# Performance work log

Measured on AMD Instinct MI355X. Metric: run time of the kernel, lower is better.

The kernel has to match this reference:

```python
import jax, jax.numpy as jnp
import numpy as np

B, D_IN, D_H, D_OUT, E = 8192, 512, 2048, 512, 8


def setup_inputs() -> dict:
    key = jax.random.key(0)
    k = jax.random.split(key, 6)
    return {
        "x": jax.random.normal(k[0], (B, D_IN), dtype=jnp.float32),
        "groups": jax.random.randint(k[1], (B, 1), 0, E, dtype=jnp.int64),
        "W1": jax.random.normal(k[2], (E, D_IN, D_H), dtype=jnp.float32) * (1.0 / np.sqrt(D_IN)),
        "b1": jnp.zeros((E, D_H), dtype=jnp.float32),
        "W2": jax.random.normal(k[3], (E, D_H, D_OUT), dtype=jnp.float32) * (1.0 / np.sqrt(D_H)),
        "b2": jnp.zeros((E, D_OUT), dtype=jnp.float32),
    }


def reference(x, groups, W1, b1, W2, b2):
    # SubnetGate: hard one-hot routing on group column 0, then weighted
    # combine (gate value is exactly 1.0 for the selected expert).
    n_expert = W1.shape[0]
    gate = jax.nn.one_hot(groups[:, 0], n_expert, dtype=x.dtype)  # [B, E]
    out = jnp.zeros((x.shape[0], W2.shape[-1]), dtype=x.dtype)
    # Loop over the small fixed expert set (structurally distinct subnets);
    # mask-combine reproduces dispatch -> subnet -> scatter/combine exactly.
    for e in range(n_expert):
        h = jax.nn.relu(x @ W1[e] + b1[e])        # [B, D_H]
        y = h @ W2[e] + b2[e]                      # [B, D_OUT]
        out = out + gate[:, e:e + 1] * y
    return out
```

## Files before the change

kernel.cpp:

```cpp
#include <hip/hip_runtime.h>
#include <hip/hip_bf16.h>

typedef unsigned short u16;
typedef __bf16 bf16x8 __attribute__((ext_vector_type(8)));
typedef float floatx4 __attribute__((ext_vector_type(4)));
typedef unsigned short ushort8 __attribute__((ext_vector_type(8)));

#define GLOBAL_AS(p) ((const __attribute__((address_space(1))) void*)(p))
#define LDS_AS(p) ((__attribute__((address_space(3))) void*)(p))

constexpr int NB = 8192;
constexpr int DIN = 512;
constexpr int DH = 2048;
constexpr int DOUT = 512;
constexpr int NEXP = 8;
constexpr int ROWCAP = NB + NEXP * 128;
constexpr int RCAPRD = NB + NEXP * 256;
constexpr int TILE = 8192;

__device__ __forceinline__ u16 f2bf(float f) {
    unsigned u = __builtin_bit_cast(unsigned, f);
    unsigned r = u + 0x7FFFu + ((u >> 16) & 1u);
    return (u16)(r >> 16);
}

__device__ __forceinline__ int slot_off(int row, int kl) {
    return row * 64 + ((((kl >> 3) ^ (row & 7)) << 3) | (kl & 7));
}

__global__ __launch_bounds__(1024) void route_kernel(
        const int* __restrict__ groups, int* __restrict__ cnt,
        int* __restrict__ offs, int* __restrict__ perm, int* __restrict__ rpos) {
    __shared__ int wc[NEXP * 16];
    __shared__ int lcur[NEXP * 16];
    int t = threadIdx.x;
    int w = t >> 6;
    if (t < NEXP * 16) wc[t] = 0;
    __syncthreads();
    for (int i = t; i < NB; i += 1024) atomicAdd(&wc[groups[i] * 16 + w], 1);
    __syncthreads();
    if (t == 0) {
        int run = 0;
        for (int e = 0; e < NEXP; ++e) {
            offs[e] = run;
            int s = run;
            for (int j = 0; j < 16; ++j) { lcur[e * 16 + j] = s; s += wc[e * 16 + j]; }
            cnt[e] = s - run;
            run += (((s - run) + 127) >> 7) << 7;
        }
    }
    __syncthreads();
    for (int i = t; i < NB; i += 1024) {
        int e = groups[i];
        int pos = atomicAdd(&lcur[e * 16 + w], 1);
        perm[pos] = i;
        rpos[i] = pos;
    }
}

__global__ __launch_bounds__(256) void prep_kernel(
        const float* __restrict__ x, const float* __restrict__ W1,
        const float* __restrict__ W2, const int* __restrict__ rpos,
        u16* __restrict__ xsT, u16* __restrict__ w1tT, u16* __restrict__ w2tT) {
    int bx = blockIdx.x;
    int t = threadIdx.x;
    if (bx < 4096) {
        __shared__ float tile[64][65];
        bool isW1 = bx < 2048;
        int b = isW1 ? bx : bx - 2048;
        int e = b >> 8;
        int q = b & 255;
        int C = isW1 ? DH : DOUT;
        int NTP = C >> 7;
        int KTP = isW1 ? (DIN >> 6) : (DH >> 6);
        int rt = isW1 ? (q >> 5) : (q >> 3);
        int ct = isW1 ? (q & 31) : (q & 7);
        const float* s = (isW1 ? W1 : W2) + (size_t)e * (isW1 ? DIN * DH : DH * DOUT);
        u16* d = isW1 ? w1tT : w2tT;
        int r0 = rt * 64, c0 = ct * 64;
        for (int i = 0; i < 4; ++i) {
            int r = (t >> 4) + i * 16;
            int c = (t & 15) * 4;
            const float4 v = *(const float4*)&s[(size_t)(r0 + r) * C + c0 + c];
            tile[r][c] = v.x; tile[r][c + 1] = v.y; tile[r][c + 2] = v.z; tile[r][c + 3] = v.w;
        }
        __syncthreads();
        for (int i = 0; i < 2; ++i) {
            int c = (t >> 3) + i * 32;
            int r = (t & 7) * 8;
            int n = c0 + c, k = r0 + r;
            ushort8 o;
#pragma unroll
            for (int j = 0; j < 8; ++j) o[j] = f2bf(tile[r + j][c]);
            size_t off = ((size_t)(e * NTP + (n >> 7)) * KTP + (k >> 6)) * TILE
                         + slot_off(n & 127, k & 63);
            *(ushort8*)&d[off] = o;
        }
    } else {
        int r = t >> 6, lane = t & 63;
        int i = (bx - 4096) * 4 + r;
        int pos = rpos[i];
        int k = lane * 8;
        const float4 a = *(const float4*)&x[(size_t)i * DIN + k];
        const float4 b = *(const float4*)&x[(size_t)i * DIN + k + 4];
        ushort8 o;
        o[0] = f2bf(a.x); o[1] = f2bf(a.y); o[2] = f2bf(a.z); o[3] = f2bf(a.w);
        o[4] = f2bf(b.x); o[5] = f2bf(b.y); o[6] = f2bf(b.z); o[7] = f2bf(b.w);
        int lp = pos & 127;
        size_t off = (size_t)(pos >> 7) * 8 * TILE + (size_t)(k >> 6) * TILE
                     + slot_off(lp, k & 63);
        *(ushort8*)&xsT[off] = o;
    }
}


#define LDF(base, row, c0) \
    (*(const bf16x8*)&(base)[(row) * 64 + ((((c0) ^ ((row) & 7))) << 3)])

__device__ __forceinline__ void stage3(const u16* a0, const u16* a1, const u16* b,
                                       u16* buf, int soff, int doff) {
    __builtin_amdgcn_global_load_lds(GLOBAL_AS(a0 + soff), LDS_AS(buf + doff), 16, 0, 0);
    __builtin_amdgcn_global_load_lds(GLOBAL_AS(a0 + 4096 + soff), LDS_AS(buf + 4096 + doff), 16, 0, 0);
    __builtin_amdgcn_global_load_lds(GLOBAL_AS(a1 + soff), LDS_AS(buf + TILE + doff), 16, 0, 0);
    __builtin_amdgcn_global_load_lds(GLOBAL_AS(a1 + 4096 + soff), LDS_AS(buf + TILE + 4096 + doff), 16, 0, 0);
    __builtin_amdgcn_global_load_lds(GLOBAL_AS(b + soff), LDS_AS(buf + 2 * TILE + doff), 16, 0, 0);
    __builtin_amdgcn_global_load_lds(GLOBAL_AS(b + 4096 + soff), LDS_AS(buf + 2 * TILE + 4096 + doff), 16, 0, 0);
}

__device__ __forceinline__ void compute_step(const u16* At, const u16* Bt,
                                             int arow, int brow,
                                             floatx4 (&acc)[4][4], int q, int li) {
#pragma unroll
    for (int s = 0; s < 2; ++s) {
        int c0 = s * 4 + q;
        bf16x8 bfr[4];
#pragma unroll
        for (int fn = 0; fn < 4; ++fn) bfr[fn] = LDF(Bt, brow + fn * 16 + li, c0);
#pragma unroll
        for (int fm = 0; fm < 4; ++fm) {
            bf16x8 af = LDF(At, arow + fm * 16 + li, c0);
#pragma unroll
            for (int fn = 0; fn < 4; ++fn)
                acc[fm][fn] = __builtin_amdgcn_mfma_f32_16x16x32_bf16(
                    af, bfr[fn], acc[fm][fn], 0, 0, 0);
        }
    }
}

template <int KT>
__device__ __forceinline__ void gemm_core3(const u16* a0, const u16* a1, const u16* b0,
                                           u16* sm, floatx4 (&acc)[4][4],
                                           int aslot, int arow, int brow,
                                           int q, int li, int soff, int doff) {
    stage3(a0, a1, b0, sm, soff, doff);
    stage3(a0 + TILE, a1 + TILE, b0 + TILE, sm + 3 * TILE, soff, doff);
    int cur = 0;
#pragma unroll 1
    for (int kt = 0; kt < KT; ++kt) {
        if (kt + 2 < KT) {
            int nb = cur + 2; if (nb >= 3) nb -= 3;
            stage3(a0 + (size_t)(kt + 2) * TILE, a1 + (size_t)(kt + 2) * TILE,
                   b0 + (size_t)(kt + 2) * TILE, sm + (size_t)nb * 3 * TILE, soff, doff);
            asm volatile("s_waitcnt vmcnt(12)" ::: "memory");
        } else if (kt + 1 < KT) {
            asm volatile("s_waitcnt vmcnt(6)" ::: "memory");
        } else {
            asm volatile("s_waitcnt vmcnt(0)" ::: "memory");
        }
        __builtin_amdgcn_s_barrier();
        __builtin_amdgcn_sched_barrier(0);
        const u16* At = sm + (size_t)(cur * 3 + aslot) * TILE;
        const u16* Bt = sm + (size_t)(cur * 3 + 2) * TILE;
        compute_step(At, Bt, arow, brow, acc, q, li);
        __builtin_amdgcn_s_barrier();
        cur = (cur == 2) ? 0 : cur + 1;
    }
}

__global__ __launch_bounds__(512) __attribute__((amdgpu_waves_per_eu(2)))
void gemm_a(const u16* __restrict__ At, const u16* __restrict__ Bt,
            const float* __restrict__ bias, u16* __restrict__ hsT,
            const int* __restrict__ cnt, const int* __restrict__ offs) {
    __shared__ u16 sm[3 * 3 * TILE];
    int bx = blockIdx.x;
    int e = bx & 7;
    int r = bx >> 3;
    int nt = r & 15;
    int mt0 = r >> 4;
    int count = cnt[e];
    int base128 = offs[e] >> 7;
    int tid = threadIdx.x;
    int w = tid >> 6, l = tid & 63, q = l >> 4, li = l & 15;
    int wm = w >> 1, wn = w & 1;
    int aslot = wm >> 1, arow = (wm & 1) * 64, brow = wn * 64;
    int soff = tid * 8, doff = w * 512;
#pragma unroll 1
    for (int mt = mt0; mt * 256 < count; mt += 5) {
        const u16* a0 = At + (size_t)((base128 + mt * 2 + 0) * 8) * TILE;
        const u16* a1 = At + (size_t)((base128 + mt * 2 + 1) * 8) * TILE;
        const u16* b0 = Bt + (size_t)((e * 16 + nt) * 8) * TILE;
        floatx4 acc[4][4];
#pragma unroll
        for (int a = 0; a < 4; ++a)
#pragma unroll
            for (int b = 0; b < 4; ++b) acc[a][b] = (floatx4)0.0f;

        gemm_core3<8>(a0, a1, b0, sm, acc, aslot, arow, brow, q, li, soff, doff);

        float bv[4];
#pragma unroll
        for (int fn = 0; fn < 4; ++fn)
            bv[fn] = bias[(size_t)e * DH + nt * 128 + wn * 64 + fn * 16 + li];
        u16* img = sm + (size_t)w * 4096;
#pragma unroll
        for (int fm = 0; fm < 4; ++fm)
#pragma unroll
            for (int fn = 0; fn < 4; ++fn)
#pragma unroll
                for (int rr = 0; rr < 4; ++rr) {
                    float v = acc[fm][fn][rr] + bv[fn];
                    v = v > 0.0f ? v : 0.0f;
                    int row = fm * 16 + q * 4 + rr;
                    int col = fn * 16 + li;
                    img[row * 64 + ((((col >> 3) ^ (row & 7)) << 3) | (col & 7))] = f2bf(v);
                }
        if ((mt * 2 + aslot) * 128 < count) {
            u16* dst = hsT + ((size_t)(base128 + mt * 2 + aslot) * 32 + nt * 2 + wn) * TILE
                       + (wm & 1) * 4096;
#pragma unroll
            for (int j = 0; j < 8; ++j)
                *(ushort8*)&dst[j * 512 + l * 8] = *(const ushort8*)&img[j * 512 + l * 8];
        }
        __syncthreads();
    }
}

__global__ __launch_bounds__(512) __attribute__((amdgpu_waves_per_eu(2)))
void gemm_b(const u16* __restrict__ At, const u16* __restrict__ Bt,
            float* __restrict__ ps, const int* __restrict__ cnt,
            const int* __restrict__ offs) {
    __shared__ u16 sm[3 * 3 * TILE];
    int bx = blockIdx.x;
    int e = bx & 7;
    int r = bx >> 3;
    int nt = r & 3;
    int ks = (r >> 2) & 1;
    int mt0 = r >> 3;
    int count = cnt[e];
    int seg = offs[e];
    int base128 = seg >> 7;
    int tid = threadIdx.x;
    int w = tid >> 6, l = tid & 63, q = l >> 4, li = l & 15;
    int wm = w >> 1, wn = w & 1;
    int aslot = wm >> 1, arow = (wm & 1) * 64, brow = wn * 64;
    int soff = tid * 8, doff = w * 512;
#pragma unroll 1
    for (int mt = mt0; mt * 256 < count; mt += 5) {
        const u16* a0 = At + (size_t)((base128 + mt * 2 + 0) * 32 + ks * 16) * TILE;
        const u16* a1 = At + (size_t)((base128 + mt * 2 + 1) * 32 + ks * 16) * TILE;
        const u16* b0 = Bt + (size_t)((e * 4 + nt) * 32 + ks * 16) * TILE;
        floatx4 acc[4][4];
#pragma unroll
        for (int a = 0; a < 4; ++a)
#pragma unroll
            for (int b = 0; b < 4; ++b) acc[a][b] = (floatx4)0.0f;

        gemm_core3<16>(a0, a1, b0, sm, acc, aslot, arow, brow, q, li, soff, doff);

        if ((mt * 2 + aslot) * 128 < count) {
            float* pbase = ps + ((size_t)ks * ROWCAP + seg + (size_t)mt * 256) * DOUT;
#pragma unroll
            for (int fn = 0; fn < 4; ++fn) {
                int col = nt * 128 + wn * 64 + fn * 16 + li;
#pragma unroll
                for (int fm = 0; fm < 4; ++fm) {
                    int row0 = wm * 64 + fm * 16 + q * 4;
#pragma unroll
                    for (int rr = 0; rr < 4; ++rr)
                        pbase[(size_t)(row0 + rr) * DOUT + col] = acc[fm][fn][rr];
                }
            }
        }
        __syncthreads();
    }
}

__global__ __launch_bounds__(256) void reduce_b(
        const float* __restrict__ ps, const int* __restrict__ rpos,
        const int* __restrict__ groups, const float* __restrict__ b2,
        float* __restrict__ out) {
    int idx = blockIdx.x * 256 + threadIdx.x;
    int i = idx >> 7;
    int c = (idx & 127) * 4;
    int pos = rpos[i];
    int g = groups[i];
    const float4 v0 = *(const float4*)&ps[(size_t)pos * DOUT + c];
    const float4 v1 = *(const float4*)&ps[((size_t)ROWCAP + pos) * DOUT + c];
    const float4 bb = *(const float4*)&b2[(size_t)g * DOUT + c];
    float4 o;
    o.x = v0.x + v1.x + bb.x; o.y = v0.y + v1.y + bb.y;
    o.z = v0.z + v1.z + bb.z; o.w = v0.w + v1.w + bb.w;
    *(float4*)&out[(size_t)i * DOUT + c] = o;
}

extern "C" void kernel_launch(void* const* d_in, const int* in_sizes, int n_in,
                              void* d_out, int out_size, void* d_ws, size_t ws_size,
                              hipStream_t stream) {
    const float* x = (const float*)d_in[0];
    const int* groups = (const int*)d_in[1];
    const float* W1 = (const float*)d_in[2];
    const float* b1 = (const float*)d_in[3];
    const float* W2 = (const float*)d_in[4];
    const float* b2 = (const float*)d_in[5];
    float* out = (float*)d_out;

    char* ws = (char*)d_ws;
    size_t o = 0;
    auto alloc = [&](size_t bytes) {
        void* p = ws + o;
        o = (o + bytes + 255) & ~(size_t)255;
        return p;
    };
    int* cnt = (int*)alloc(NEXP * 4);
    int* offs = (int*)alloc(NEXP * 4);
    int* perm = (int*)alloc((size_t)ROWCAP * 4);
    int* rpos = (int*)alloc((size_t)NB * 4);
    u16* xsT = (u16*)alloc((size_t)(RCAPRD / 128) * 8 * TILE * 2);
    u16* w1tT = (u16*)alloc((size_t)NEXP * DIN * DH * 2);
    u16* w2tT = (u16*)alloc((size_t)NEXP * DH * DOUT * 2);
    u16* hsT = (u16*)alloc((size_t)(RCAPRD / 128) * 32 * TILE * 2);
    float* ps = (float*)alloc((size_t)2 * ROWCAP * DOUT * 4);

    route_kernel<<<1, 1024, 0, stream>>>(groups, cnt, offs, perm, rpos);
    prep_kernel<<<6144, 256, 0, stream>>>(x, W1, W2, rpos, xsT, w1tT, w2tT);
    gemm_a<<<NEXP * 16 * 5, 512, 0, stream>>>(xsT, w1tT, b1, hsT, cnt, offs);
    gemm_b<<<NEXP * 4 * 2 * 5, 512, 0, stream>>>(hsT, w2tT, ps, cnt, offs);
    reduce_b<<<(NB * (DOUT / 4)) / 256, 256, 0, stream>>>(ps, rpos, groups, b2, out);
}
```

Baseline: 220.1 us.

## Shrink GEMM tiles to 128x128 with 256 threads and double-buffered LDS

Both grouped GEMM kernels go from 256x128 tiles with 512 threads and a three-stage LDS pipeline to 128x128 tiles with 256 threads and a two-stage double buffer. The next stage is issued after the barrier, and the grid grows from 5 to 9 m-tile strides per (expert, n-tile). Smaller tiles and less LDS should let more blocks run per CU and spread work across more blocks. The cost is less B-tile reuse per block, a shallower prefetch that waits on vmcnt(0) every step, and dropped tail guards that now rely on padded buffers. The output store guard is also removed.

```diff
diff --git a/kernel.cpp b/kernel.cpp
--- a/kernel.cpp
+++ b/kernel.cpp
@@ -117,14 +117,15 @@
 #define LDF(base, row, c0) \
     (*(const bf16x8*)&(base)[(row) * 64 + ((((c0) ^ ((row) & 7))) << 3)])
 
-__device__ __forceinline__ void stage3(const u16* a0, const u16* a1, const u16* b,
+__device__ __forceinline__ void stage2(const u16* a, const u16* b,
                                        u16* buf, int soff, int doff) {
-    __builtin_amdgcn_global_load_lds(GLOBAL_AS(a0 + soff), LDS_AS(buf + doff), 16, 0, 0);
-    __builtin_amdgcn_global_load_lds(GLOBAL_AS(a0 + 4096 + soff), LDS_AS(buf + 4096 + doff), 16, 0, 0);
-    __builtin_amdgcn_global_load_lds(GLOBAL_AS(a1 + soff), LDS_AS(buf + TILE + doff), 16, 0, 0);
-    __builtin_amdgcn_global_load_lds(GLOBAL_AS(a1 + 4096 + soff), LDS_AS(buf + TILE + 4096 + doff), 16, 0, 0);
-    __builtin_amdgcn_global_load_lds(GLOBAL_AS(b + soff), LDS_AS(buf + 2 * TILE + doff), 16, 0, 0);
-    __builtin_amdgcn_global_load_lds(GLOBAL_AS(b + 4096 + soff), LDS_AS(buf + 2 * TILE + 4096 + doff), 16, 0, 0);
+#pragma unroll
+    for (int ch = 0; ch < 4; ++ch) {
+        __builtin_amdgcn_global_load_lds(GLOBAL_AS(a + ch * 2048 + soff),
+                                         LDS_AS(buf + ch * 2048 + doff), 16, 0, 0);
+        __builtin_amdgcn_global_load_lds(GLOBAL_AS(b + ch * 2048 + soff),
+                                         LDS_AS(buf + TILE + ch * 2048 + doff), 16, 0, 0);
+    }
 }
 
 __device__ __forceinline__ void compute_step(const u16* At, const u16* Bt,
@@ -148,40 +149,34 @@
 }
 
 template <int KT>
-__device__ __forceinline__ void gemm_core3(const u16* a0, const u16* a1, const u16* b0,
+__device__ __forceinline__ void gemm_core2(const u16* a0, const u16* b0,
                                            u16* sm, floatx4 (&acc)[4][4],
-                                           int aslot, int arow, int brow,
+                                           int arow, int brow,
                                            int q, int li, int soff, int doff) {
-    stage3(a0, a1, b0, sm, soff, doff);
-    stage3(a0 + TILE, a1 + TILE, b0 + TILE, sm + 3 * TILE, soff, doff);
+    stage2(a0, b0, sm, soff, doff);
     int cur = 0;
 #pragma unroll 1
     for (int kt = 0; kt < KT; ++kt) {
-        if (kt + 2 < KT) {
-            int nb = cur + 2; if (nb >= 3) nb -= 3;
-            stage3(a0 + (size_t)(kt + 2) * TILE, a1 + (size_t)(kt + 2) * TILE,
-                   b0 + (size_t)(kt + 2) * TILE, sm + (size_t)nb * 3 * TILE, soff, doff);
-            asm volatile("s_waitcnt vmcnt(12)" ::: "memory");
-        } else if (kt + 1 < KT) {
-            asm volatile("s_waitcnt vmcnt(6)" ::: "memory");
-        } else {
-            asm volatile("s_waitcnt vmcnt(0)" ::: "memory");
-        }
+        asm volatile("s_waitcnt vmcnt(0)" ::: "memory");
         __builtin_amdgcn_s_barrier();
         __builtin_amdgcn_sched_barrier(0);
-        const u16* At = sm + (size_t)(cur * 3 + aslot) * TILE;
-        const u16* Bt = sm + (size_t)(cur * 3 + 2) * TILE;
+        if (kt + 1 < KT)
+            stage2(a0 + (size_t)(kt + 1) * TILE, b0 + (size_t)(kt + 1) * TILE,
+                   sm + (size_t)(cur ^ 1) * 2 * TILE, soff, doff);
+        const u16* At = sm + (size_t)(cur * 2 + 0) * TILE;
+        const u16* Bt = sm + (size_t)(cur * 2 + 1) * TILE;
         compute_step(At, Bt, arow, brow, acc, q, li);
+        __builtin_amdgcn_sched_barrier(0);
         __builtin_amdgcn_s_barrier();
-        cur = (cur == 2) ? 0 : cur + 1;
-    }
-}
-
-__global__ __launch_bounds__(512) __attribute__((amdgpu_waves_per_eu(2)))
+        cur ^= 1;
+    }
+}
+
+__global__ __launch_bounds__(256) __attribute__((amdgpu_waves_per_eu(2)))
 void gemm_a(const u16* __restrict__ At, const u16* __restrict__ Bt,
             const float* __restrict__ bias, u16* __restrict__ hsT,
             const int* __restrict__ cnt, const int* __restrict__ offs) {
-    __shared__ u16 sm[3 * 3 * TILE];
+    __shared__ u16 sm[2 * 2 * TILE];
     int bx = blockIdx.x;
     int e = bx & 7;
     int r = bx >> 3;
@@ -192,12 +187,11 @@
     int tid = threadIdx.x;
     int w = tid >> 6, l = tid & 63, q = l >> 4, li = l & 15;
     int wm = w >> 1, wn = w & 1;
-    int aslot = wm >> 1, arow = (wm & 1) * 64, brow = wn * 64;
+    int arow = wm * 64, brow = wn * 64;
     int soff = tid * 8, doff = w * 512;
 #pragma unroll 1
-    for (int mt = mt0; mt * 256 < count; mt += 5) {
-        const u16* a0 = At + (size_t)((base128 + mt * 2 + 0) * 8) * TILE;
-        const u16* a1 = At + (size_t)((base128 + mt * 2 + 1) * 8) * TILE;
+    for (int mt = mt0; mt * 128 < count; mt += 9) {
+        const u16* a0 = At + (size_t)((base128 + mt) * 8) * TILE;
         const u16* b0 = Bt + (size_t)((e * 16 + nt) * 8) * TILE;
         floatx4 acc[4][4];
 #pragma unroll
@@ -205,7 +199,7 @@
 #pragma unroll
             for (int b = 0; b < 4; ++b) acc[a][b] = (floatx4)0.0f;
 
-        gemm_core3<8>(a0, a1, b0, sm, acc, aslot, arow, brow, q, li, soff, doff);
+        gemm_core2<8>(a0, b0, sm, acc, arow, brow, q, li, soff, doff);
 
         float bv[4];
 #pragma unroll
@@ -224,22 +218,19 @@
                     int col = fn * 16 + li;
                     img[row * 64 + ((((col >> 3) ^ (row & 7)) << 3) | (col & 7))] = f2bf(v);
                 }
-        if ((mt * 2 + aslot) * 128 < count) {
-            u16* dst = hsT + ((size_t)(base128 + mt * 2 + aslot) * 32 + nt * 2 + wn) * TILE
-                       + (wm & 1) * 4096;
-#pragma unroll
-            for (int j = 0; j < 8; ++j)
-                *(ushort8*)&dst[j * 512 + l * 8] = *(const ushort8*)&img[j * 512 + l * 8];
-        }
+        u16* dst = hsT + ((size_t)(base128 + mt) * 32 + nt * 2 + wn) * TILE + wm * 4096;
+#pragma unroll
+        for (int j = 0; j < 8; ++j)
+            *(ushort8*)&dst[j * 512 + l * 8] = *(const ushort8*)&img[j * 512 + l * 8];
         __syncthreads();
     }
 }
 
-__global__ __launch_bounds__(512) __attribute__((amdgpu_waves_per_eu(2)))
+__global__ __launch_bounds__(256) __attribute__((amdgpu_waves_per_eu(2)))
 void gemm_b(const u16* __restrict__ At, const u16* __restrict__ Bt,
             float* __restrict__ ps, const int* __restrict__ cnt,
             const int* __restrict__ offs) {
-    __shared__ u16 sm[3 * 3 * TILE];
+    __shared__ u16 sm[2 * 2 * TILE];
     int bx = blockIdx.x;
     int e = bx & 7;
     int r = bx >> 3;
@@ -252,12 +243,11 @@
     int tid = threadIdx.x;
     int w = tid >> 6, l = tid & 63, q = l >> 4, li = l & 15;
     int wm = w >> 1, wn = w & 1;
-    int aslot = wm >> 1, arow = (wm & 1) * 64, brow = wn * 64;
+    int arow = wm * 64, brow = wn * 64;
     int soff = tid * 8, doff = w * 512;
 #pragma unroll 1
-    for (int mt = mt0; mt * 256 < count; mt += 5) {
-        const u16* a0 = At + (size_t)((base128 + mt * 2 + 0) * 32 + ks * 16) * TILE;
-        const u16* a1 = At + (size_t)((base128 + mt * 2 + 1) * 32 + ks * 16) * TILE;
+    for (int mt = mt0; mt * 128 < count; mt += 9) {
+        const u16* a0 = At + (size_t)((base128 + mt) * 32 + ks * 16) * TILE;
         const u16* b0 = Bt + (size_t)((e * 4 + nt) * 32 + ks * 16) * TILE;
         floatx4 acc[4][4];
 #pragma unroll
@@ -265,20 +255,18 @@
 #pragma unroll
             for (int b = 0; b < 4; ++b) acc[a][b] = (floatx4)0.0f;
 
-        gemm_core3<16>(a0, a1, b0, sm, acc, aslot, arow, brow, q, li, soff, doff);
-
-        if ((mt * 2 + aslot) * 128 < count) {
-            float* pbase = ps + ((size_t)ks * ROWCAP + seg + (size_t)mt * 256) * DOUT;
-#pragma unroll
-            for (int fn = 0; fn < 4; ++fn) {
-                int col = nt * 128 + wn * 64 + fn * 16 + li;
-#pragma unroll
-                for (int fm = 0; fm < 4; ++fm) {
-                    int row0 = wm * 64 + fm * 16 + q * 4;
-#pragma unroll
-                    for (int rr = 0; rr < 4; ++rr)
-                        pbase[(size_t)(row0 + rr) * DOUT + col] = acc[fm][fn][rr];
-                }
+        gemm_core2<16>(a0, b0, sm, acc, arow, brow, q, li, soff, doff);
+
+        float* pbase = ps + ((size_t)ks * ROWCAP + seg + (size_t)mt * 128) * DOUT;
+#pragma unroll
+        for (int fn = 0; fn < 4; ++fn) {
+            int col = nt * 128 + wn * 64 + fn * 16 + li;
+#pragma unroll
+            for (int fm = 0; fm < 4; ++fm) {
+                int row0 = wm * 64 + fm * 16 + q * 4;
+#pragma unroll
+                for (int rr = 0; rr < 4; ++rr)
+                    pbase[(size_t)(row0 + rr) * DOUT + col] = acc[fm][fn][rr];
             }
         }
         __syncthreads();
@@ -333,7 +321,7 @@
 
     route_kernel<<<1, 1024, 0, stream>>>(groups, cnt, offs, perm, rpos);
     prep_kernel<<<6144, 256, 0, stream>>>(x, W1, W2, rpos, xsT, w1tT, w2tT);
-    gemm_a<<<NEXP * 16 * 5, 512, 0, stream>>>(xsT, w1tT, b1, hsT, cnt, offs);
-    gemm_b<<<NEXP * 4 * 2 * 5, 512, 0, stream>>>(hsT, w2tT, ps, cnt, offs);
+    gemm_a<<<NEXP * 16 * 9, 256, 0, stream>>>(xsT, w1tT, b1, hsT, cnt, offs);
+    gemm_b<<<NEXP * 4 * 2 * 9, 256, 0, stream>>>(hsT, w2tT, ps, cnt, offs);
     reduce_b<<<(NB * (DOUT / 4)) / 256, 256, 0, stream>>>(ps, rpos, groups, b2, out);
 }
```

Result: faster. 206.0 us (-6.4%).
